# Kernel tuning notes

Hardware: AMD Instinct MI355X
Metric: run time of the kernel (lower is better)

## Reference

```python
import jax, jax.numpy as jnp
import numpy as np

B, C, H, W = 4, 3, 1024, 1024


def softsplat_sum(im, flow):
    """Summation forward-warp (softsplat, no metric): bilinear scatter-add.
    im: [B,C,H,W], flow: [B,2,H,W] (flow[:,0]=dx, flow[:,1]=dy)."""
    b, c, h, w = im.shape
    n = h * w
    X = jnp.arange(w, dtype=flow.dtype)[None, None, :] + flow[:, 0]  # [B,H,W]
    Y = jnp.arange(h, dtype=flow.dtype)[None, :, None] + flow[:, 1]  # [B,H,W]
    x0 = jnp.floor(X); y0 = jnp.floor(Y)
    x1 = x0 + 1.0;     y1 = y0 + 1.0
    # bilinear weights for the 4 surrounding integer pixels: NW, NE, SW, SE
    ws = jnp.stack([(x1 - X) * (y1 - Y), (X - x0) * (y1 - Y),
                    (x1 - X) * (Y - y0), (X - x0) * (Y - y0)])  # [4,B,H,W]
    xi = jnp.stack([x0, x1, x0, x1]).astype(jnp.int32)
    yi = jnp.stack([y0, y0, y1, y1]).astype(jnp.int32)
    valid = (xi >= 0) & (xi < w) & (yi >= 0) & (yi < h)
    ws = jnp.where(valid, ws, 0.0)
    idx = jnp.clip(yi, 0, h - 1) * w + jnp.clip(xi, 0, w - 1)     # [4,B,H,W]
    idx = idx.reshape(4, b, n).transpose(1, 0, 2)                  # [B,4,N]
    ws = ws.reshape(4, b, n).transpose(1, 0, 2)                    # [B,4,N]
    imf = im.reshape(b, c, n)

    def splat_one(imf_b, idx_b, w_b):
        vals = (imf_b[:, None, :] * w_b[None]).reshape(c, 4 * n)   # [C,4N]
        return jnp.zeros((c, n), imf_b.dtype).at[:, idx_b.reshape(-1)].add(vals)

    out = jax.vmap(splat_one)(imf, idx, ws)                        # [B,C,N]
    return out.reshape(b, c, h, w)


def setup_inputs() -> dict:
    key = jax.random.key(0)
    k1, k2, k3, k4 = jax.random.split(key, 4)
    flows = 5.0 * jax.random.normal(k1, (2, B, 2, H, W), jnp.float32)
    im0 = jax.random.uniform(k2, (B, C, H, W), jnp.float32)
    im1 = jax.random.uniform(k3, (B, C, H, W), jnp.float32)
    t_value = 0.2 + 0.6 * jax.random.uniform(k4, (B,), jnp.float32)
    return {"flows": flows, "im0": im0, "im1": im1, "t_value": t_value}


def reference(flows, im0, im1, t_value):
    t = t_value.reshape(-1, 1, 1, 1)
    warped_fir = softsplat_sum(im0, (1.0 / t) * flows[0])
    warped_sec = softsplat_sum(im1, (1.0 / (1.0 - t)) * flows[1])
    loss = jnp.mean(jnp.abs(warped_fir - im1)) + jnp.mean(jnp.abs(warped_sec - im0))
    return loss
```

## Files before the change

kernel.cpp:

```cpp
#include <hip/hip_runtime.h>

#define BN 4
#define CN 3
#define HN 1024
#define WN 1024
#define HW (HN * WN)
#define BHW (BN * HW)
#define TOT (BN * CN * HW)

#define TS 64
#define TXN (WN / TS)
#define TYN (HN / TS)
#define NTB (TXN * TYN)
#define NTILE (BN * NTB)
#define CAP 8192
#define CHUNK 1024
#define NCHB (BHW / CHUNK)
#define NPAIR (CHUNK / 512)

#define OFF_GCNT 0
#define OFF_BORD 4096
#define SZ_BORD  (BN * 16 * 1024 * 8)
#define OFF_LOSS (OFF_BORD + 4 * SZ_BORD)
#define OFF_REC  (OFF_LOSS + 256)
#define WS_NEED  ((size_t)OFF_REC + (size_t)NTILE * CAP * 8)

#define BSCALE 65536.0f
#define INV_BSCALE (1.0f / 65536.0f)
#define FMASK 0x1FFFFFull

#define PQ 252.0f
#define INV_PQ (1.0f / 252.0f)
#define VQ 4095.0f
#define VSCL (65536.0f / 4095.0f)

__device__ __forceinline__ float blockReduce4(float local, float* smem) {
#pragma unroll
    for (int off = 32; off > 0; off >>= 1)
        local += __shfl_down(local, off, 64);
    int wave = threadIdx.x >> 6;
    if ((threadIdx.x & 63) == 0) smem[wave] = local;
    __syncthreads();
    float s = 0.0f;
    if (threadIdx.x == 0)
        s = smem[0] + smem[1] + smem[2] + smem[3];
    return s;
}

__global__ __launch_bounds__(256) void p1_kernel(
    const float* __restrict__ flow,
    const float* __restrict__ im,
    const float* __restrict__ tv,
    unsigned int* __restrict__ gcnt,
    unsigned long long* __restrict__ rec,
    int invert)
{
    __shared__ unsigned int cnt[NTB];
    __shared__ unsigned int off[NTB];
    __shared__ unsigned int sexc[NTB];
    __shared__ unsigned long long stage[CHUNK];
    int tid = threadIdx.x;
    cnt[tid] = 0;
    __syncthreads();

    int base = blockIdx.x * CHUNK;
    int b = base >> 20;
    int pb = base - b * HW;
    float t = tv[b];
    float s = invert ? (1.0f / (1.0f - t)) : (1.0f / t);
    const float2* fxp = (const float2*)(flow + (size_t)(b * 2 + 0) * HW);
    const float2* fyp = (const float2*)(flow + (size_t)(b * 2 + 1) * HW);
    const float2* v0p = (const float2*)(im + (size_t)(b * 3 + 0) * HW);
    const float2* v1p = (const float2*)(im + (size_t)(b * 3 + 1) * HW);
    const float2* v2p = (const float2*)(im + (size_t)(b * 3 + 2) * HW);

    unsigned sc[2 * NPAIR];
    unsigned long long pay[2 * NPAIR];

#pragma unroll
    for (int i = 0; i < NPAIR; ++i) {
        int p0 = pb + 2 * tid + i * 512;
        int y = p0 >> 10;
        int x = p0 & 1023;
        int e = p0 >> 1;
        float2 fx2 = fxp[e], fy2 = fyp[e];
        float2 c02 = v0p[e], c12 = v1p[e], c22 = v2p[e];
        float Xh[2], Yh[2], vv0[2], vv1[2], vv2[2];
        Xh[0] = (float)x + s * fx2.x;        Xh[1] = (float)(x + 1) + s * fx2.y;
        Yh[0] = (float)y + s * fy2.x;        Yh[1] = (float)y + s * fy2.y;
        vv0[0] = c02.x; vv0[1] = c02.y;
        vv1[0] = c12.x; vv1[1] = c12.y;
        vv2[0] = c22.x; vv2[1] = c22.y;
        int kk[2]; bool val[2];
#pragma unroll
        for (int h = 0; h < 2; ++h) {
            int x0 = (int)floorf(Xh[h]);
            int y0 = (int)floorf(Yh[h]);
            val[h] = !(x0 < -1 || x0 > WN - 1 || y0 < -1 || y0 > HN - 1);
            int bx = (x0 < 0 ? 0 : x0) >> 6;
            int by = (y0 < 0 ? 0 : y0) >> 6;
            kk[h] = (by << 4) + bx;
            float lx = Xh[h] - (float)(bx << 6);
            float ly = Yh[h] - (float)(by << 6);
            unsigned long long lq = __float2uint_rn((lx + 1.0f) * PQ);
            unsigned long long mq = __float2uint_rn((ly + 1.0f) * PQ);
            unsigned long long q0 = __float2uint_rn(vv0[h] * VQ);
            unsigned long long q1 = __float2uint_rn(vv1[h] * VQ);
            unsigned long long q2 = __float2uint_rn(vv2[h] * VQ);
            pay[2 * i + h] = lq | (mq << 14) | (q0 << 28) | (q1 << 40) | (q2 << 52);
        }
        if (val[0] & val[1] & (kk[0] == kk[1])) {
            unsigned ls = atomicAdd(&cnt[kk[0]], 2u);
            sc[2 * i]     = ((unsigned)kk[0] << 16) | ls;
            sc[2 * i + 1] = ((unsigned)kk[0] << 16) | (ls + 1u);
        } else {
            sc[2 * i]     = val[0] ? (((unsigned)kk[0] << 16) | atomicAdd(&cnt[kk[0]], 1u))
                                   : 0xFFFFFFFFu;
            sc[2 * i + 1] = val[1] ? (((unsigned)kk[1] << 16) | atomicAdd(&cnt[kk[1]], 1u))
                                   : 0xFFFFFFFFu;
        }
    }
    __syncthreads();

    unsigned c = cnt[tid];
    unsigned g = c ? atomicAdd(&gcnt[b * NTB + tid], c) : 0u;
    if (tid < 64) {
        unsigned v0 = cnt[4 * tid], v1 = cnt[4 * tid + 1];
        unsigned v2 = cnt[4 * tid + 2], v3 = cnt[4 * tid + 3];
        unsigned s01 = v0 + v1;
        unsigned tot = s01 + v2 + v3;
        unsigned run = tot;
#pragma unroll
        for (int d = 1; d < 64; d <<= 1) {
            unsigned u = __shfl_up(run, d, 64);
            if (tid >= d) run += u;
        }
        unsigned excl = run - tot;
        sexc[4 * tid]     = excl;
        sexc[4 * tid + 1] = excl + v0;
        sexc[4 * tid + 2] = excl + s01;
        sexc[4 * tid + 3] = excl + s01 + v2;
    }
    off[tid] = g;
    __syncthreads();

#pragma unroll
    for (int j = 0; j < 2 * NPAIR; ++j) {
        unsigned scv = sc[j];
        if (scv == 0xFFFFFFFFu) continue;
        stage[sexc[scv >> 16] + (scv & 0xFFFFu)] = pay[j];
    }
    __syncthreads();

    int wave = tid >> 6, lane = tid & 63;
    for (int k2 = wave; k2 < NTB; k2 += 4) {
        unsigned c2 = cnt[k2];
        if (!c2) continue;
        unsigned gb = off[k2];
        if (gb >= CAP) continue;
        if (gb + c2 > CAP) c2 = CAP - gb;
        unsigned sb = sexc[k2];
        unsigned long long* dst = rec + (size_t)(b * NTB + k2) * CAP + gb;
        for (unsigned j2 = lane; j2 < c2; j2 += 64)
            dst[j2] = stage[sb + j2];
    }
}

__global__ __launch_bounds__(256) void p2_kernel(
    const unsigned long long* __restrict__ rec,
    unsigned int* __restrict__ gcnt,
    const float* __restrict__ ref,
    unsigned long long* __restrict__ rowacc,
    unsigned long long* __restrict__ colacc,
    double* __restrict__ loss)
{
    __shared__ unsigned long long tileu[65 * 65];
    __shared__ float smem4[4];
    int k = blockIdx.x;
    int b  = k >> 8;
    int by = (k >> 4) & 15;
    int bx = k & 15;
    int tx = bx << 6, ty = by << 6;
    int tid = threadIdx.x;

    for (int i = tid; i < 65 * 65; i += 256) tileu[i] = 0ull;
    __syncthreads();

    unsigned n = gcnt[k];
    if (n > CAP) n = CAP;
    const unsigned long long* rk = rec + (size_t)k * CAP;
    for (unsigned r = tid; r < n; r += 256) {
        unsigned long long w = rk[r];
        float lx = (float)(unsigned)(w & 0x3FFFu)         * INV_PQ - 1.0f;
        float ly = (float)(unsigned)((w >> 14) & 0x3FFFu) * INV_PQ - 1.0f;
        float v0s = (float)(unsigned)((w >> 28) & 0xFFFu) * VSCL;
        float v1s = (float)(unsigned)((w >> 40) & 0xFFFu) * VSCL;
        float v2s = (float)(unsigned)((w >> 52) & 0xFFFu) * VSCL;
        int i0 = (int)floorf(lx); if (i0 > 63) i0 = 63;
        int j0 = (int)floorf(ly); if (j0 > 63) j0 = 63;
        float fx = lx - (float)i0;
        float fy = ly - (float)j0;
        float wx0 = 1.0f - fx, wy0 = 1.0f - fy;
#pragma unroll
        for (int c = 0; c < 4; ++c) {
            int ii = i0 + (c & 1), jj = j0 + (c >> 1);
            float w4 = (c & 1 ? fx : wx0) * (c >> 1 ? fy : wy0);
            if (ii >= 0 && jj >= 0 && tx + ii < WN && ty + jj < HN) {
                unsigned long long pk =
                      (unsigned long long)__float2uint_rn(v0s * w4)
                    | ((unsigned long long)__float2uint_rn(v1s * w4) << 21)
                    | ((unsigned long long)__float2uint_rn(v2s * w4) << 42);
                atomicAdd(&tileu[jj * 65 + ii], pk);
            }
        }
    }
    __syncthreads();
    if (tid == 0) gcnt[k] = 0;

    float local = 0.0f;
    for (int c = tid; c < 65 * 65; c += 256) {
        int j = c / 65, i = c - j * 65;
        int gx = tx + i, gy = ty + j;
        if (gx >= WN || gy >= HN) continue;
        unsigned long long a = tileu[c];
        bool fin_i = (i >= 1 || bx == 0) && (i <= 63);
        bool fin_j = (j >= 1 || by == 0) && (j <= 63);
        if (fin_i && fin_j) {
            float a0 = (float)(unsigned)(a & FMASK)         * INV_BSCALE;
            float a1 = (float)(unsigned)((a >> 21) & FMASK) * INV_BSCALE;
            float a2 = (float)(unsigned)((a >> 42) & FMASK) * INV_BSCALE;
            size_t o = (size_t)gy * WN + gx;
            local += fabsf(a0 - ref[(size_t)(b * 3 + 0) * HW + o])
                   + fabsf(a1 - ref[(size_t)(b * 3 + 1) * HW + o])
                   + fabsf(a2 - ref[(size_t)(b * 3 + 2) * HW + o]);
        } else if (a) {
            if ((gy & 63) == 0 && gy >= 64)
                atomicAdd(&rowacc[((size_t)(b * 16 + (gy >> 6)) << 10) + gx], a);
            else
                atomicAdd(&colacc[((size_t)(b * 16 + (gx >> 6)) << 10) + gy], a);
        }
    }
    float ssum = blockReduce4(local, smem4);
    if (tid == 0) unsafeAtomicAdd(loss, (double)ssum);
}

__global__ __launch_bounds__(256) void border_kernel(
    const unsigned long long* __restrict__ bord,
    const float* __restrict__ ref0,
    const float* __restrict__ ref1,
    double* __restrict__ loss)
{
    __shared__ float smem4[4];
    int idx = blockIdx.x * 256 + threadIdx.x;
    int reg = idx >> 16;
    int e = idx & 0xFFFF;
    bool isrow = (reg & 1) == 0;
    const float* ref = (reg < 2) ? ref0 : ref1;
    unsigned long long a = bord[idx];
    int b = e >> 14;
    int rc = (e >> 10) & 15;
    int q = e & 1023;
    float local = 0.0f;
    bool process;
    int gx, gy;
    if (isrow) { process = (rc >= 1); gy = rc << 6; gx = q; }
    else       { process = (rc >= 1) && !(((q & 63) == 0) && q >= 64); gx = rc << 6; gy = q; }
    if (process && a) {
        float a0 = (float)(unsigned)(a & FMASK)         * INV_BSCALE;
        float a1 = (float)(unsigned)((a >> 21) & FMASK) * INV_BSCALE;
        float a2 = (float)(unsigned)((a >> 42) & FMASK) * INV_BSCALE;
        size_t o = (size_t)gy * WN + gx;
        local += fabsf(a0 - ref[(size_t)(b * 3 + 0) * HW + o])
               + fabsf(a1 - ref[(size_t)(b * 3 + 1) * HW + o])
               + fabsf(a2 - ref[(size_t)(b * 3 + 2) * HW + o]);
    } else if (process) {
        size_t o = (size_t)gy * WN + gx;
        local += fabsf(ref[(size_t)(b * 3 + 0) * HW + o])
               + fabsf(ref[(size_t)(b * 3 + 1) * HW + o])
               + fabsf(ref[(size_t)(b * 3 + 2) * HW + o]);
    }
    float ssum = blockReduce4(local, smem4);
    if (threadIdx.x == 0) unsafeAtomicAdd(loss, (double)ssum);
}

__global__ void finalize_kernel(const double* __restrict__ loss,
                                float* __restrict__ out)
{
    out[0] = (float)(loss[0] / (double)TOT);
}

#define FPSCALE 65536.0f
#define INV_FPSCALE (1.0f / 65536.0f)

__device__ __forceinline__ unsigned long long pack3f(float c0, float c1, float c2, float w) {
    unsigned long long f0 = (unsigned long long)__float2uint_rn(c0 * w * FPSCALE);
    unsigned long long f1 = (unsigned long long)__float2uint_rn(c1 * w * FPSCALE);
    unsigned long long f2 = (unsigned long long)__float2uint_rn(c2 * w * FPSCALE);
    return f0 | (f1 << 21) | (f2 << 42);
}

__global__ __launch_bounds__(256) void splat_kernel(
    const float* __restrict__ flow, const float* __restrict__ im,
    const float* __restrict__ tv, unsigned long long* __restrict__ acc, int invert)
{
    int gid = blockIdx.x * blockDim.x + threadIdx.x;
    if (gid >= BHW) return;
    int b = gid / HW;
    int p = gid - b * HW;
    int y = p >> 10, x = p & 1023;
    float t = tv[b];
    float s = invert ? (1.0f / (1.0f - t)) : (1.0f / t);
    float X = (float)x + s * flow[(size_t)(b * 2 + 0) * HW + p];
    float Y = (float)y + s * flow[(size_t)(b * 2 + 1) * HW + p];
    float x0f = floorf(X), y0f = floorf(Y);
    int x0 = (int)x0f, y0 = (int)y0f;
    float fx = X - x0f, fy = Y - y0f;
    float wx0 = 1.0f - fx, wx1 = fx, wy0 = 1.0f - fy, wy1 = fy;
    float v0 = im[(size_t)(b * 3 + 0) * HW + p];
    float v1 = im[(size_t)(b * 3 + 1) * HW + p];
    float v2 = im[(size_t)(b * 3 + 2) * HW + p];
    bool vx0 = (x0 >= 0) & (x0 < WN);
    bool vx1 = (x0 + 1 >= 0) & (x0 + 1 < WN);
    unsigned long long* accb = acc + (size_t)b * HW;
#pragma unroll
    for (int r = 0; r < 2; ++r) {
        int yi = y0 + r;
        if (yi < 0 || yi >= HN) continue;
        float wy = r ? wy1 : wy0;
        size_t rowbase = (size_t)yi * WN;
        if (vx0) atomicAdd(&accb[rowbase + x0],     pack3f(v0, v1, v2, wx0 * wy));
        if (vx1) atomicAdd(&accb[rowbase + x0 + 1], pack3f(v0, v1, v2, wx1 * wy));
    }
}

__global__ __launch_bounds__(256) void loss_kernel(
    unsigned long long* __restrict__ acc, const float* __restrict__ ref,
    double* __restrict__ loss)
{
    __shared__ float smem4[4];
    int stride = gridDim.x * blockDim.x;
    float local = 0.0f;
    for (int i = blockIdx.x * blockDim.x + threadIdx.x; i < BHW; i += stride) {
        int b = i / HW;
        int p = i - b * HW;
        unsigned long long a = acc[i];
        acc[i] = 0ull;
        float c0 = (float)(unsigned)(a & FMASK)         * INV_FPSCALE;
        float c1 = (float)(unsigned)((a >> 21) & FMASK) * INV_FPSCALE;
        float c2 = (float)(unsigned)((a >> 42) & FMASK) * INV_FPSCALE;
        local += fabsf(c0 - ref[(size_t)(b * 3 + 0) * HW + p])
               + fabsf(c1 - ref[(size_t)(b * 3 + 1) * HW + p])
               + fabsf(c2 - ref[(size_t)(b * 3 + 2) * HW + p]);
    }
    float ssum = blockReduce4(local, smem4);
    if (threadIdx.x == 0) unsafeAtomicAdd(loss, (double)ssum);
}

extern "C" void kernel_launch(void* const* d_in, const int* in_sizes, int n_in,
                              void* d_out, int out_size, void* d_ws, size_t ws_size,
                              hipStream_t stream)
{
    const float* flows = (const float*)d_in[0];
    const float* im0   = (const float*)d_in[1];
    const float* im1   = (const float*)d_in[2];
    const float* tv    = (const float*)d_in[3];
    const float* flows1 = flows + (size_t)BN * 2 * HW;
    const int threads = 256;

    if (ws_size >= WS_NEED) {
        char* ws = (char*)d_ws;
        unsigned int* gcnt = (unsigned int*)(ws + OFF_GCNT);
        unsigned long long* bord = (unsigned long long*)(ws + OFF_BORD);
        unsigned long long* row0 = bord;
        unsigned long long* col0 = bord + (size_t)BN * 16 * 1024;
        unsigned long long* row1 = bord + 2 * (size_t)BN * 16 * 1024;
        unsigned long long* col1 = bord + 3 * (size_t)BN * 16 * 1024;
        double* loss = (double*)(ws + OFF_LOSS);
        unsigned long long* rec = (unsigned long long*)(ws + OFF_REC);

        hipMemsetAsync(d_ws, 0, OFF_REC, stream);

        p1_kernel<<<NCHB, threads, 0, stream>>>(flows, im0, tv, gcnt, rec, 0);
        p2_kernel<<<NTILE, threads, 0, stream>>>(rec, gcnt, im1, row0, col0, loss);

        p1_kernel<<<NCHB, threads, 0, stream>>>(flows1, im1, tv, gcnt, rec, 1);
        p2_kernel<<<NTILE, threads, 0, stream>>>(rec, gcnt, im0, row1, col1, loss);

        border_kernel<<<1024, threads, 0, stream>>>(bord, im1, im0, loss);
        finalize_kernel<<<1, 1, 0, stream>>>(loss, (float*)d_out);
    } else {
        unsigned long long* acc = (unsigned long long*)d_ws;
        double* loss = (double*)(acc + (size_t)BN * HW);
        hipMemsetAsync(d_ws, 0, sizeof(unsigned long long) * (size_t)BN * HW + sizeof(double), stream);
        const int sgrid = (BHW + threads - 1) / threads;
        splat_kernel<<<sgrid, threads, 0, stream>>>(flows, im0, tv, acc, 0);
        loss_kernel<<<2048, threads, 0, stream>>>(acc, im1, loss);
        splat_kernel<<<sgrid, threads, 0, stream>>>(flows1, im1, tv, acc, 1);
        loss_kernel<<<2048, threads, 0, stream>>>(acc, im0, loss);
        finalize_kernel<<<1, 1, 0, stream>>>(loss, (float*)d_out);
    }
}
```

Baseline: 289.5 us.

## Batch both warp directions into single binning and tile-splat launches

Merges the two forward-warp directions into one p1 launch and one p2 launch when workspace allows, which doubles the grid and removes two dependent launches. CHUNK grows to 4096 pixels per binning block. The per-bucket wave-serial copy-out is replaced by a flat per-element scatter that uses a byte bucket tag. The finalize kernel is folded into the border kernel through a last-block ticket, and the per-tile counter reset is dropped in favour of separate counters per direction. This adds workspace pressure, more shared memory per p1 block (lower occupancy), and a runtime-chosen record capacity that may truncate.

```diff
diff --git a/kernel.cpp b/kernel.cpp
--- a/kernel.cpp
+++ b/kernel.cpp
@@ -9,23 +9,21 @@
 #define TOT (BN * CN * HW)
 
 #define TS 64
-#define TXN (WN / TS)
-#define TYN (HN / TS)
-#define NTB (TXN * TYN)
-#define NTILE (BN * NTB)
-#define CAP 8192
-#define CHUNK 1024
-#define NCHB (BHW / CHUNK)
-#define NPAIR (CHUNK / 512)
+#define TXN 16
+#define TYN 16
+#define NTB 256
+#define NTILE 1024
+#define CHUNK 4096
+#define NCHB 1024
+#define NPAIR 8
 
 #define OFF_GCNT 0
-#define OFF_BORD 4096
-#define SZ_BORD  (BN * 16 * 1024 * 8)
-#define OFF_LOSS (OFF_BORD + 4 * SZ_BORD)
-#define OFF_REC  (OFF_LOSS + 256)
-#define WS_NEED  ((size_t)OFF_REC + (size_t)NTILE * CAP * 8)
-
-#define BSCALE 65536.0f
+#define OFF_LOSS 8192
+#define OFF_TICK 8200
+#define OFF_BORD 8448
+#define SZ_BORDR (BN * 16 * 1024 * 8)
+#define OFF_REC  (OFF_BORD + 4 * SZ_BORDR)
+
 #define INV_BSCALE (1.0f / 65536.0f)
 #define FMASK 0x1FFFFFull
 
@@ -48,26 +46,40 @@
 }
 
 __global__ __launch_bounds__(256) void p1_kernel(
-    const float* __restrict__ flow,
-    const float* __restrict__ im,
+    const float* __restrict__ flows,
+    const float* __restrict__ im0,
+    const float* __restrict__ im1,
     const float* __restrict__ tv,
     unsigned int* __restrict__ gcnt,
     unsigned long long* __restrict__ rec,
-    int invert)
+    int cap, int dirsel)
 {
     __shared__ unsigned int cnt[NTB];
     __shared__ unsigned int off[NTB];
     __shared__ unsigned int sexc[NTB];
+    __shared__ unsigned int stot;
+    __shared__ unsigned char sbkt[CHUNK];
     __shared__ unsigned long long stage[CHUNK];
     int tid = threadIdx.x;
     cnt[tid] = 0;
     __syncthreads();
 
-    int base = blockIdx.x * CHUNK;
+    int bid = blockIdx.x;
+    int dir, chunk;
+    if (dirsel == 2) { dir = bid >> 10; chunk = bid & 1023; }
+    else             { dir = dirsel;    chunk = bid; }
+
+    const float* flow = flows + (size_t)dir * (BN * 2 * HW);
+    const float* im   = dir ? im1 : im0;
+    unsigned int* gk  = gcnt + dir * NTILE;
+    unsigned long long* recd =
+        rec + (size_t)((dirsel == 2) ? dir : 0) * NTILE * (size_t)cap;
+
+    int base = chunk * CHUNK;
     int b = base >> 20;
     int pb = base - b * HW;
     float t = tv[b];
-    float s = invert ? (1.0f / (1.0f - t)) : (1.0f / t);
+    float s = dir ? (1.0f / (1.0f - t)) : (1.0f / t);
     const float2* fxp = (const float2*)(flow + (size_t)(b * 2 + 0) * HW);
     const float2* fyp = (const float2*)(flow + (size_t)(b * 2 + 1) * HW);
     const float2* v0p = (const float2*)(im + (size_t)(b * 3 + 0) * HW);
@@ -123,7 +135,7 @@
     __syncthreads();
 
     unsigned c = cnt[tid];
-    unsigned g = c ? atomicAdd(&gcnt[b * NTB + tid], c) : 0u;
+    unsigned g = c ? atomicAdd(&gk[b * NTB + tid], c) : 0u;
     if (tid < 64) {
         unsigned v0 = cnt[4 * tid], v1 = cnt[4 * tid + 1];
         unsigned v2 = cnt[4 * tid + 2], v3 = cnt[4 * tid + 3];
@@ -140,6 +152,7 @@
         sexc[4 * tid + 1] = excl + v0;
         sexc[4 * tid + 2] = excl + s01;
         sexc[4 * tid + 3] = excl + s01 + v2;
+        if (tid == 63) stot = run;
     }
     off[tid] = g;
     __syncthreads();
@@ -148,35 +161,43 @@
     for (int j = 0; j < 2 * NPAIR; ++j) {
         unsigned scv = sc[j];
         if (scv == 0xFFFFFFFFu) continue;
-        stage[sexc[scv >> 16] + (scv & 0xFFFFu)] = pay[j];
-    }
-    __syncthreads();
-
-    int wave = tid >> 6, lane = tid & 63;
-    for (int k2 = wave; k2 < NTB; k2 += 4) {
-        unsigned c2 = cnt[k2];
-        if (!c2) continue;
-        unsigned gb = off[k2];
-        if (gb >= CAP) continue;
-        if (gb + c2 > CAP) c2 = CAP - gb;
-        unsigned sb = sexc[k2];
-        unsigned long long* dst = rec + (size_t)(b * NTB + k2) * CAP + gb;
-        for (unsigned j2 = lane; j2 < c2; j2 += 64)
-            dst[j2] = stage[sb + j2];
+        unsigned k = scv >> 16;
+        unsigned pos = sexc[k] + (scv & 0xFFFFu);
+        stage[pos] = pay[j];
+        sbkt[pos] = (unsigned char)k;
+    }
+    __syncthreads();
+
+    unsigned T = stot;
+    for (unsigned j = tid; j < T; j += 256) {
+        int k2 = sbkt[j];
+        unsigned slot = off[k2] + (j - sexc[k2]);
+        if (slot < (unsigned)cap)
+            recd[(size_t)(b * NTB + k2) * (size_t)cap + slot] = stage[j];
     }
 }
 
 __global__ __launch_bounds__(256) void p2_kernel(
     const unsigned long long* __restrict__ rec,
-    unsigned int* __restrict__ gcnt,
-    const float* __restrict__ ref,
-    unsigned long long* __restrict__ rowacc,
-    unsigned long long* __restrict__ colacc,
-    double* __restrict__ loss)
+    const unsigned int* __restrict__ gcnt,
+    const float* __restrict__ im0,
+    const float* __restrict__ im1,
+    unsigned long long* __restrict__ bord,
+    double* __restrict__ loss,
+    int cap, int dirsel)
 {
     __shared__ unsigned long long tileu[65 * 65];
     __shared__ float smem4[4];
-    int k = blockIdx.x;
+    int kb = blockIdx.x;
+    int dir, k;
+    if (dirsel == 2) { dir = kb >> 10; k = kb & 1023; }
+    else             { dir = dirsel;   k = kb; }
+    const float* ref = dir ? im0 : im1;
+    const unsigned long long* recd =
+        rec + (size_t)((dirsel == 2) ? dir : 0) * NTILE * (size_t)cap;
+    unsigned long long* rowacc = bord + (size_t)(2 * dir)     * (BN * 16 * 1024);
+    unsigned long long* colacc = bord + (size_t)(2 * dir + 1) * (BN * 16 * 1024);
+
     int b  = k >> 8;
     int by = (k >> 4) & 15;
     int bx = k & 15;
@@ -186,9 +207,9 @@
     for (int i = tid; i < 65 * 65; i += 256) tileu[i] = 0ull;
     __syncthreads();
 
-    unsigned n = gcnt[k];
-    if (n > CAP) n = CAP;
-    const unsigned long long* rk = rec + (size_t)k * CAP;
+    unsigned n = gcnt[dir * NTILE + k];
+    if (n > (unsigned)cap) n = cap;
+    const unsigned long long* rk = recd + (size_t)k * (size_t)cap;
     for (unsigned r = tid; r < n; r += 256) {
         unsigned long long w = rk[r];
         float lx = (float)(unsigned)(w & 0x3FFFu)         * INV_PQ - 1.0f;
@@ -215,7 +236,6 @@
         }
     }
     __syncthreads();
-    if (tid == 0) gcnt[k] = 0;
 
     float local = 0.0f;
     for (int c = tid; c < 65 * 65; c += 256) {
@@ -248,7 +268,9 @@
     const unsigned long long* __restrict__ bord,
     const float* __restrict__ ref0,
     const float* __restrict__ ref1,
-    double* __restrict__ loss)
+    double* __restrict__ loss,
+    unsigned int* __restrict__ ticket,
+    float* __restrict__ out)
 {
     __shared__ float smem4[4];
     int idx = blockIdx.x * 256 + threadIdx.x;
@@ -280,13 +302,15 @@
                + fabsf(ref[(size_t)(b * 3 + 2) * HW + o]);
     }
     float ssum = blockReduce4(local, smem4);
-    if (threadIdx.x == 0) unsafeAtomicAdd(loss, (double)ssum);
-}
-
-__global__ void finalize_kernel(const double* __restrict__ loss,
-                                float* __restrict__ out)
-{
-    out[0] = (float)(loss[0] / (double)TOT);
+    if (threadIdx.x == 0) {
+        unsafeAtomicAdd(loss, (double)ssum);
+        __threadfence();
+        unsigned tkt = atomicAdd(ticket, 1u);
+        if (tkt == gridDim.x - 1) {
+            double v = unsafeAtomicAdd(loss, 0.0);
+            out[0] = (float)(v / (double)TOT);
+        }
+    }
 }
 
 #define FPSCALE 65536.0f
@@ -356,6 +380,12 @@
     if (threadIdx.x == 0) unsafeAtomicAdd(loss, (double)ssum);
 }
 
+__global__ void finalize_kernel(const double* __restrict__ loss,
+                                float* __restrict__ out)
+{
+    out[0] = (float)(loss[0] / (double)TOT);
+}
+
 extern "C" void kernel_launch(void* const* d_in, const int* in_sizes, int n_in,
                               void* d_out, int out_size, void* d_ws, size_t ws_size,
                               hipStream_t stream)
@@ -367,36 +397,51 @@
     const float* flows1 = flows + (size_t)BN * 2 * HW;
     const int threads = 256;
 
-    if (ws_size >= WS_NEED) {
-        char* ws = (char*)d_ws;
-        unsigned int* gcnt = (unsigned int*)(ws + OFF_GCNT);
-        unsigned long long* bord = (unsigned long long*)(ws + OFF_BORD);
-        unsigned long long* row0 = bord;
-        unsigned long long* col0 = bord + (size_t)BN * 16 * 1024;
-        unsigned long long* row1 = bord + 2 * (size_t)BN * 16 * 1024;
-        unsigned long long* col1 = bord + 3 * (size_t)BN * 16 * 1024;
-        double* loss = (double*)(ws + OFF_LOSS);
-        unsigned long long* rec = (unsigned long long*)(ws + OFF_REC);
-
+    long long avail = (long long)ws_size - (long long)OFF_REC;
+    int capBoth = 0, capSeq = 0;
+    if (avail > 0) {
+        long long cb = avail / (2LL * NTILE * 8);
+        long long cs = avail / ((long long)NTILE * 8);
+        capBoth = (int)(cb > 8192 ? 8192 : cb);
+        capSeq  = (int)(cs > 8192 ? 8192 : cs);
+    }
+
+    char* ws = (char*)d_ws;
+    unsigned int* gcnt = (unsigned int*)(ws + OFF_GCNT);
+    double* loss = (double*)(ws + OFF_LOSS);
+    unsigned int* ticket = (unsigned int*)(ws + OFF_TICK);
+    unsigned long long* bord = (unsigned long long*)(ws + OFF_BORD);
+    unsigned long long* rec = (unsigned long long*)(ws + OFF_REC);
+
+    if (capBoth >= 5120) {
         hipMemsetAsync(d_ws, 0, OFF_REC, stream);
-
-        p1_kernel<<<NCHB, threads, 0, stream>>>(flows, im0, tv, gcnt, rec, 0);
-        p2_kernel<<<NTILE, threads, 0, stream>>>(rec, gcnt, im1, row0, col0, loss);
-
-        p1_kernel<<<NCHB, threads, 0, stream>>>(flows1, im1, tv, gcnt, rec, 1);
-        p2_kernel<<<NTILE, threads, 0, stream>>>(rec, gcnt, im0, row1, col1, loss);
-
-        border_kernel<<<1024, threads, 0, stream>>>(bord, im1, im0, loss);
-        finalize_kernel<<<1, 1, 0, stream>>>(loss, (float*)d_out);
+        p1_kernel<<<2 * NCHB, threads, 0, stream>>>(flows, im0, im1, tv,
+                                                    gcnt, rec, capBoth, 2);
+        p2_kernel<<<2 * NTILE, threads, 0, stream>>>(rec, gcnt, im0, im1,
+                                                     bord, loss, capBoth, 2);
+        border_kernel<<<1024, threads, 0, stream>>>(bord, im1, im0, loss,
+                                                    ticket, (float*)d_out);
+    } else if (capSeq >= 5120) {
+        hipMemsetAsync(d_ws, 0, OFF_REC, stream);
+        p1_kernel<<<NCHB, threads, 0, stream>>>(flows, im0, im1, tv,
+                                                gcnt, rec, capSeq, 0);
+        p2_kernel<<<NTILE, threads, 0, stream>>>(rec, gcnt, im0, im1,
+                                                 bord, loss, capSeq, 0);
+        p1_kernel<<<NCHB, threads, 0, stream>>>(flows, im0, im1, tv,
+                                                gcnt, rec, capSeq, 1);
+        p2_kernel<<<NTILE, threads, 0, stream>>>(rec, gcnt, im0, im1,
+                                                 bord, loss, capSeq, 1);
+        border_kernel<<<1024, threads, 0, stream>>>(bord, im1, im0, loss,
+                                                    ticket, (float*)d_out);
     } else {
         unsigned long long* acc = (unsigned long long*)d_ws;
-        double* loss = (double*)(acc + (size_t)BN * HW);
+        double* lss = (double*)(acc + (size_t)BN * HW);
         hipMemsetAsync(d_ws, 0, sizeof(unsigned long long) * (size_t)BN * HW + sizeof(double), stream);
         const int sgrid = (BHW + threads - 1) / threads;
         splat_kernel<<<sgrid, threads, 0, stream>>>(flows, im0, tv, acc, 0);
-        loss_kernel<<<2048, threads, 0, stream>>>(acc, im1, loss);
+        loss_kernel<<<2048, threads, 0, stream>>>(acc, im1, lss);
         splat_kernel<<<sgrid, threads, 0, stream>>>(flows1, im1, tv, acc, 1);
-        loss_kernel<<<2048, threads, 0, stream>>>(acc, im0, loss);
-        finalize_kernel<<<1, 1, 0, stream>>>(loss, (float*)d_out);
-    }
-}
+        loss_kernel<<<2048, threads, 0, stream>>>(acc, im0, lss);
+        finalize_kernel<<<1, 1, 0, stream>>>(lss, (float*)d_out);
+    }
+}
```

Measured after the change: 296.9 us. 1.03x slower.
